# Kernel optimization log

Hardware: AMD Instinct MI355X
Metric: run time of the kernel (lower is better)

The kernel has to match this reference:

```python
import jax, jax.numpy as jnp
import numpy as np

IN_CH = 128
OUT_CH = 128
N_NODES = 50000
N_EDGES = 800000
BN_EPS = 1e-5


def setup_inputs() -> dict:
    key = jax.random.key(0)
    k_x, k_e, k_wl, k_bl, k_wr = jax.random.split(key, 5)
    x = jax.random.normal(k_x, (N_NODES, IN_CH), dtype=jnp.float32)
    edge_index = jax.random.randint(k_e, (2, N_EDGES), 0, N_NODES, dtype=jnp.int64)
    s = 1.0 / np.sqrt(IN_CH)
    W_l = jax.random.uniform(k_wl, (OUT_CH, IN_CH), jnp.float32, -s, s)  # lin_l: aggregated neighbors
    b_l = jax.random.uniform(k_bl, (OUT_CH,), jnp.float32, -s, s)
    W_r = jax.random.uniform(k_wr, (OUT_CH, IN_CH), jnp.float32, -s, s)  # lin_r: root/self
    gamma = jnp.ones((OUT_CH,), jnp.float32)
    beta = jnp.zeros((OUT_CH,), jnp.float32)
    return {"x": x, "edge_index": edge_index, "W_l": W_l, "b_l": b_l,
            "W_r": W_r, "gamma": gamma, "beta": beta}


def reference(x, edge_index, W_l, b_l, W_r, gamma, beta):
    n = x.shape[0]
    src, dst = edge_index[0], edge_index[1]
    # gather source features and mean-aggregate at destination nodes
    msgs = x[src]                                              # [E, C_in]
    agg = jax.ops.segment_sum(msgs, dst, num_segments=n)      # [N, C_in]
    deg = jax.ops.segment_sum(jnp.ones((edge_index.shape[1],), x.dtype), dst, num_segments=n)
    mean_agg = agg / jnp.maximum(deg, 1.0)[:, None]
    # SAGEConv: lin_l(aggregated) + lin_r(self)
    h = mean_agg @ W_l.T + b_l + x @ W_r.T                     # [N, C_out]
    # BatchNorm1d (training-mode batch statistics, biased variance)
    mu = h.mean(axis=0)
    var = ((h - mu) ** 2).mean(axis=0)
    h = (h - mu) * jax.lax.rsqrt(var + BN_EPS) * gamma + beta
    return jax.nn.relu(h)
```

## Files before the change

kernel.cpp:

```cpp
#include <hip/hip_runtime.h>

#define CH 128
#define BN_EPS 1e-5f

typedef unsigned int uint32;
typedef unsigned short ushort16;
using f32x2  = __attribute__((ext_vector_type(2))) float;
using f32x4  = __attribute__((ext_vector_type(4))) float;
using bf16x8 = __attribute__((ext_vector_type(8))) short;

__device__ __forceinline__ ushort16 f2b(float f) {
    uint32 u = __float_as_uint(f);
    return (ushort16)((u + 0x7FFFu + ((u >> 16) & 1u)) >> 16);
}
__device__ __forceinline__ uint32 pk2(float a, float b) {
    return (uint32)f2b(a) | ((uint32)f2b(b) << 16);
}
__device__ __forceinline__ float blo(uint32 u) { return __uint_as_float(u << 16); }
__device__ __forceinline__ float bhi(uint32 u) { return __uint_as_float(u & 0xFFFF0000u); }

__global__ __launch_bounds__(256) void sage_init(
    const float* __restrict__ Wl, const float* __restrict__ Wr,
    int* __restrict__ head, ushort16* __restrict__ wct,
    float* __restrict__ bn, uint32* __restrict__ xqz, int nNodes)
{
    int i = blockIdx.x * 256 + threadIdx.x;
    if (i < nNodes) head[i] = -1;
    if (blockIdx.x < 128) {
        int widx = blockIdx.x * 256 + threadIdx.x;
        int co = widx >> 8, k = widx & 255;
        float v = (k < 128) ? Wr[co * 128 + k] : Wl[co * 128 + (k - 128)];
        wct[widx] = f2b(v);
    }
    if (blockIdx.x == 0) bn[threadIdx.x] = 0.f;
    if (blockIdx.x == 1 && threadIdx.x < 32) xqz[threadIdx.x] = 0;
}

__global__ __launch_bounds__(256) void sage_prep(
    const float* __restrict__ x, const void* __restrict__ ei,
    int* __restrict__ head, int2* __restrict__ pair,
    uint32* __restrict__ xb4, uint2* __restrict__ xq8,
    int nEdges, int total8)
{
    const int* pi = (const int*)ei;
    int lane = threadIdx.x & 63;
    bool is64 = (__ballot(pi[lane * 2 + 1] != 0) == 0ULL);

    int idx = blockIdx.x * 256 + threadIdx.x;
    bool hasE = (idx < nEdges);
    bool hasC = (idx < total8);

    int s = 0, d = 0;
    if (hasE) {
        if (is64) {
            const long long* p = (const long long*)ei;
            s = (int)p[idx];
            d = (int)p[nEdges + idx];
        } else {
            s = pi[idx];
            d = pi[nEdges + idx];
        }
    }
    const float4* x4 = (const float4*)x;
    float4 a = make_float4(0, 0, 0, 0), b = make_float4(0, 0, 0, 0);
    if (hasC) { a = x4[2 * idx]; b = x4[2 * idx + 1]; }

    int old = 0;
    if (hasE) old = atomicExch(&head[d], idx);

    if (hasC) {
        uint4 o;
        o.x = pk2(a.x, a.y); o.y = pk2(a.z, a.w);
        o.z = pk2(b.x, b.y); o.w = pk2(b.z, b.w);
        ((uint4*)xb4)[idx] = o;

        int qa = __builtin_amdgcn_cvt_pk_fp8_f32(a.x, a.y, 0, false);
        qa = __builtin_amdgcn_cvt_pk_fp8_f32(a.z, a.w, qa, true);
        int qb = __builtin_amdgcn_cvt_pk_fp8_f32(b.x, b.y, 0, false);
        qb = __builtin_amdgcn_cvt_pk_fp8_f32(b.z, b.w, qb, true);
        xq8[idx] = make_uint2((uint32)qa, (uint32)qb);
    }

    if (hasE) pair[idx] = make_int2(old, s);
}

__global__ __launch_bounds__(256) void sage_aggregate(
    const char* __restrict__ xq, const int* __restrict__ head,
    const int2* __restrict__ pair, uint32* __restrict__ mean_b, int nNodes)
{
    int wid = blockIdx.x * 4 + (threadIdx.x >> 6);
    int nbase = wid * 8;
    if (nbase >= nNodes) return;
    int lane = threadIdx.x & 63;
    int chain = lane >> 3;
    int sub = lane & 7;

    const int ZROW = nNodes;

    int cur = -1;
    if (lane < 8) {
        int n = nbase + lane;
        cur = (n < nNodes) ? head[n] : -1;
    }
    int cnt = 0;
    f32x2 acc2[8];
    #pragma unroll
    for (int i = 0; i < 8; ++i) acc2[i] = (f32x2){0.f, 0.f};

    int2 pr = make_int2(-1, ZROW);
    if (cur >= 0) pr = pair[cur];

    while (__ballot(cur >= 0) != 0ULL) {
        int nxt = pr.x;
        int2 prn = make_int2(-1, ZROW);
        if (cur >= 0 && nxt >= 0) prn = pair[nxt];

        int s = __shfl(pr.y, chain);
        uint4 u = *(const uint4*)(xq + ((size_t)s << 7) + sub * 16);
        #pragma unroll
        for (int w = 0; w < 4; ++w) {
            uint32 uw = (&u.x)[w];
            acc2[w * 2 + 0] += __builtin_amdgcn_cvt_pk_f32_fp8((int)uw, false);
            acc2[w * 2 + 1] += __builtin_amdgcn_cvt_pk_f32_fp8((int)uw, true);
        }
        if (cur >= 0) { ++cnt; cur = nxt; }
        pr = prn;
    }

    int cn = __shfl(cnt, chain);
    float inv = 1.0f / fmaxf((float)cn, 1.0f);
    int n = nbase + chain;
    if (n < nNodes) {
        uint4 o0 = make_uint4(pk2(acc2[0][0] * inv, acc2[0][1] * inv),
                              pk2(acc2[1][0] * inv, acc2[1][1] * inv),
                              pk2(acc2[2][0] * inv, acc2[2][1] * inv),
                              pk2(acc2[3][0] * inv, acc2[3][1] * inv));
        uint4 o1 = make_uint4(pk2(acc2[4][0] * inv, acc2[4][1] * inv),
                              pk2(acc2[5][0] * inv, acc2[5][1] * inv),
                              pk2(acc2[6][0] * inv, acc2[6][1] * inv),
                              pk2(acc2[7][0] * inv, acc2[7][1] * inv));
        char* base = (char*)mean_b + (size_t)n * 256 + sub * 32;
        *(uint4*)base = o0;
        *(uint4*)(base + 16) = o1;
    }
}

__global__ __launch_bounds__(256) void sage_gemm(
    const ushort16* __restrict__ xb, const ushort16* __restrict__ mean_b,
    const ushort16* __restrict__ wct, const float* __restrict__ bl,
    ushort16* __restrict__ hb, float* __restrict__ bn, int nNodes)
{
    __shared__ ushort16 wsh[8 * 8 * 64 * 8];
    __shared__ float redS[4][CH];
    __shared__ float redQ[4][CH];

    int tid = threadIdx.x;
    int wave = tid >> 6, lane = tid & 63;
    int col = lane & 15, kg = lane >> 4;

    #pragma unroll
    for (int it = 0; it < 16; ++it) {
        int pidx = wave * 16 + it;
        int cb = pidx >> 3, ks = pidx & 7;
        bf16x8 v = *(const bf16x8*)(wct + (size_t)(cb * 16 + col) * 256 + ks * 32 + kg * 8);
        *(bf16x8*)(wsh + ((size_t)pidx * 64 + lane) * 8) = v;
    }

    int row0 = blockIdx.x * 128 + wave * 16;
    int row1 = row0 + 64;
    int arow0 = min(row0 + col, nNodes - 1);
    int arow1 = min(row1 + col, nNodes - 1);
    const ushort16* xr0 = xb + (size_t)arow0 * CH;
    const ushort16* mr0 = mean_b + (size_t)arow0 * CH;
    const ushort16* xr1 = xb + (size_t)arow1 * CH;
    const ushort16* mr1 = mean_b + (size_t)arow1 * CH;

    bf16x8 af0[8], af1[8];
    #pragma unroll
    for (int t = 0; t < 4; ++t) {
        af0[t]     = *(const bf16x8*)(xr0 + t * 32 + kg * 8);
        af0[4 + t] = *(const bf16x8*)(mr0 + t * 32 + kg * 8);
        af1[t]     = *(const bf16x8*)(xr1 + t * 32 + kg * 8);
        af1[4 + t] = *(const bf16x8*)(mr1 + t * 32 + kg * 8);
    }

    __syncthreads();

    f32x4 acc0[8], acc1[8];
    #pragma unroll
    for (int cb = 0; cb < 8; ++cb) {
        acc0[cb] = (f32x4){0.f, 0.f, 0.f, 0.f};
        acc1[cb] = (f32x4){0.f, 0.f, 0.f, 0.f};
    }

    #pragma unroll
    for (int kstep = 0; kstep < 8; ++kstep) {
        #pragma unroll
        for (int cb = 0; cb < 8; ++cb) {
            bf16x8 b = *(const bf16x8*)(wsh + ((size_t)(cb * 8 + kstep) * 64 + lane) * 8);
            acc0[cb] = __builtin_amdgcn_mfma_f32_16x16x32_bf16(af0[kstep], b, acc0[cb], 0, 0, 0);
            acc1[cb] = __builtin_amdgcn_mfma_f32_16x16x32_bf16(af1[kstep], b, acc1[cb], 0, 0, 0);
        }
    }

    #pragma unroll
    for (int cb = 0; cb < 8; ++cb) {
        int co = cb * 16 + col;
        float blv = bl[co];
        float s = 0.f, ss = 0.f;
        #pragma unroll
        for (int j = 0; j < 4; ++j) {
            int r0 = row0 + kg * 4 + j;
            float v0 = acc0[cb][j] + blv;
            if (r0 < nNodes) {
                hb[(size_t)r0 * CH + co] = f2b(v0);
                s += v0; ss += v0 * v0;
            }
            int r1 = row1 + kg * 4 + j;
            float v1 = acc1[cb][j] + blv;
            if (r1 < nNodes) {
                hb[(size_t)r1 * CH + co] = f2b(v1);
                s += v1; ss += v1 * v1;
            }
        }
        s  += __shfl_xor(s, 16);  s  += __shfl_xor(s, 32);
        ss += __shfl_xor(ss, 16); ss += __shfl_xor(ss, 32);
        if (kg == 0) { redS[wave][co] = s; redQ[wave][co] = ss; }
    }
    __syncthreads();
    if (tid < CH) {
        atomicAdd(&bn[tid], redS[0][tid] + redS[1][tid] + redS[2][tid] + redS[3][tid]);
    } else {
        int c = tid - CH;
        atomicAdd(&bn[CH + c], redQ[0][c] + redQ[1][c] + redQ[2][c] + redQ[3][c]);
    }
}

__global__ __launch_bounds__(256) void sage_apply(
    const ushort16* __restrict__ hb, float* __restrict__ out,
    const float* __restrict__ bn, const float* __restrict__ gamma,
    const float* __restrict__ beta, int total8, int nNodes)
{
    __shared__ float sc_sh[CH], sh_sh[CH];
    int tid = threadIdx.x;
    if (tid < CH) {
        float invN = 1.0f / (float)nNodes;
        float mu = bn[tid] * invN;
        float var = fmaxf(bn[CH + tid] * invN - mu * mu, 0.f);
        float sc = gamma[tid] * rsqrtf(var + BN_EPS);
        sc_sh[tid] = sc;
        sh_sh[tid] = beta[tid] - mu * sc;
    }
    __syncthreads();
    int i = blockIdx.x * 256 + tid;
    if (i >= total8) return;
    uint4 u = *(const uint4*)(hb + (size_t)i * 8);
    int c = (i * 8) & 127;
    float4 o0, o1;
    o0.x = fmaxf(fmaf(blo(u.x), sc_sh[c + 0], sh_sh[c + 0]), 0.f);
    o0.y = fmaxf(fmaf(bhi(u.x), sc_sh[c + 1], sh_sh[c + 1]), 0.f);
    o0.z = fmaxf(fmaf(blo(u.y), sc_sh[c + 2], sh_sh[c + 2]), 0.f);
    o0.w = fmaxf(fmaf(bhi(u.y), sc_sh[c + 3], sh_sh[c + 3]), 0.f);
    o1.x = fmaxf(fmaf(blo(u.z), sc_sh[c + 4], sh_sh[c + 4]), 0.f);
    o1.y = fmaxf(fmaf(bhi(u.z), sc_sh[c + 5], sh_sh[c + 5]), 0.f);
    o1.z = fmaxf(fmaf(blo(u.w), sc_sh[c + 6], sh_sh[c + 6]), 0.f);
    o1.w = fmaxf(fmaf(bhi(u.w), sc_sh[c + 7], sh_sh[c + 7]), 0.f);
    float4* dst = (float4*)(out + (size_t)i * 8);
    dst[0] = o0;
    dst[1] = o1;
}

extern "C" void kernel_launch(void* const* d_in, const int* in_sizes, int n_in,
                              void* d_out, int out_size, void* d_ws, size_t ws_size,
                              hipStream_t stream)
{
    const float* x     = (const float*)d_in[0];
    const void*  ei    = d_in[1];
    const float* Wl    = (const float*)d_in[2];
    const float* bl    = (const float*)d_in[3];
    const float* Wr    = (const float*)d_in[4];
    const float* gamma = (const float*)d_in[5];
    const float* beta  = (const float*)d_in[6];

    int nNodes = in_sizes[0] / CH;
    int nEdges = in_sizes[1] / 2;
    int nBlkM  = (nNodes + 127) / 128;

    char* p = (char*)d_ws;
    auto take = [&](size_t bytes) {
        char* r = p;
        p += (bytes + 255) & ~(size_t)255;
        return r;
    };
    ushort16* xb      = (ushort16*)take((size_t)nNodes * CH * 2);
    char*     xq      = (char*)take((size_t)nNodes * CH + 128);
    ushort16* mean_b  = (ushort16*)take((size_t)nNodes * CH * 2);
    ushort16* hb      = (ushort16*)take((size_t)nNodes * CH * 2);
    ushort16* wct     = (ushort16*)take((size_t)CH * 256 * 2);
    int*      head    = (int*)take((size_t)nNodes * 4);
    float*    bn      = (float*)take(256 * 4);
    int2*     pair    = (int2*)take((size_t)nEdges * 8);

    float* out = (float*)d_out;

    int total8 = nNodes * CH / 8;
    int eBlocks = (nEdges + 255) / 256;
    int pBlocks = max(eBlocks, (total8 + 255) / 256);
    int iBlocks = max((nNodes + 255) / 256, 128);

    sage_init<<<iBlocks, 256, 0, stream>>>(
        Wl, Wr, head, wct, bn, (uint32*)(xq + (size_t)nNodes * CH), nNodes);

    sage_prep<<<pBlocks, 256, 0, stream>>>(
        x, ei, head, pair, (uint32*)xb, (uint2*)xq, nEdges, total8);

    int aBlocks = (nNodes + 31) / 32;
    sage_aggregate<<<aBlocks, 256, 0, stream>>>(
        xq, head, pair, (uint32*)mean_b, nNodes);

    sage_gemm<<<nBlkM, 256, 0, stream>>>(
        xb, mean_b, wct, bl, hb, bn, nNodes);

    sage_apply<<<(total8 + 255) / 256, 256, 0, stream>>>(
        hb, out, bn, gamma, beta, total8, nNodes);
}
```

Baseline: 113.7 us.

## Split each node's edge linked list into two chains for more memory parallelism

Edges are now pushed onto one of two per-node linked lists, picked by edge index parity, so each destination has two independent chains. The aggregate kernel walks 16 chains per wave (two per node, in A/B accumulator sets), which halves the serial pointer-chasing depth and doubles the gathers in flight. Partial sums from the two chains are combined with a cross-lane shuffle before the mean is written. This costs twice the head array, doubled accumulator registers, and some idle lanes during the final write.

```diff
diff --git a/kernel.cpp b/kernel.cpp
--- a/kernel.cpp
+++ b/kernel.cpp
@@ -22,10 +22,10 @@
 __global__ __launch_bounds__(256) void sage_init(
     const float* __restrict__ Wl, const float* __restrict__ Wr,
     int* __restrict__ head, ushort16* __restrict__ wct,
-    float* __restrict__ bn, uint32* __restrict__ xqz, int nNodes)
+    float* __restrict__ bn, uint32* __restrict__ xqz, int nHead)
 {
     int i = blockIdx.x * 256 + threadIdx.x;
-    if (i < nNodes) head[i] = -1;
+    if (i < nHead) head[i] = -1;
     if (blockIdx.x < 128) {
         int widx = blockIdx.x * 256 + threadIdx.x;
         int co = widx >> 8, k = widx & 255;
@@ -66,7 +66,7 @@
     if (hasC) { a = x4[2 * idx]; b = x4[2 * idx + 1]; }
 
     int old = 0;
-    if (hasE) old = atomicExch(&head[d], idx);
+    if (hasE) old = atomicExch(&head[(d << 1) | (idx & 1)], idx);
 
     if (hasC) {
         uint4 o;
@@ -92,20 +92,20 @@
     int nbase = wid * 8;
     if (nbase >= nNodes) return;
     int lane = threadIdx.x & 63;
-    int chain = lane >> 3;
+    int grp = lane >> 3;
     int sub = lane & 7;
 
     const int ZROW = nNodes;
 
     int cur = -1;
-    if (lane < 8) {
-        int n = nbase + lane;
-        cur = (n < nNodes) ? head[n] : -1;
+    if (lane < 16) {
+        int n = nbase + (lane >> 1);
+        if (n < nNodes) cur = head[((size_t)n << 1) | (lane & 1)];
     }
     int cnt = 0;
-    f32x2 acc2[8];
-    #pragma unroll
-    for (int i = 0; i < 8; ++i) acc2[i] = (f32x2){0.f, 0.f};
+    f32x2 aA[8], aB[8];
+    #pragma unroll
+    for (int i = 0; i < 8; ++i) { aA[i] = (f32x2){0.f, 0.f}; aB[i] = (f32x2){0.f, 0.f}; }
 
     int2 pr = make_int2(-1, ZROW);
     if (cur >= 0) pr = pair[cur];
@@ -115,33 +115,63 @@
         int2 prn = make_int2(-1, ZROW);
         if (cur >= 0 && nxt >= 0) prn = pair[nxt];
 
-        int s = __shfl(pr.y, chain);
-        uint4 u = *(const uint4*)(xq + ((size_t)s << 7) + sub * 16);
+        int sA = __shfl(pr.y, grp);
+        int sB = __shfl(pr.y, 8 + grp);
+        uint4 uA = *(const uint4*)(xq + ((size_t)sA << 7) + sub * 16);
+        uint4 uB = *(const uint4*)(xq + ((size_t)sB << 7) + sub * 16);
         #pragma unroll
         for (int w = 0; w < 4; ++w) {
-            uint32 uw = (&u.x)[w];
-            acc2[w * 2 + 0] += __builtin_amdgcn_cvt_pk_f32_fp8((int)uw, false);
-            acc2[w * 2 + 1] += __builtin_amdgcn_cvt_pk_f32_fp8((int)uw, true);
+            uint32 wA = (&uA.x)[w], wB = (&uB.x)[w];
+            aA[w * 2 + 0] += __builtin_amdgcn_cvt_pk_f32_fp8((int)wA, false);
+            aA[w * 2 + 1] += __builtin_amdgcn_cvt_pk_f32_fp8((int)wA, true);
+            aB[w * 2 + 0] += __builtin_amdgcn_cvt_pk_f32_fp8((int)wB, false);
+            aB[w * 2 + 1] += __builtin_amdgcn_cvt_pk_f32_fp8((int)wB, true);
         }
         if (cur >= 0) { ++cnt; cur = nxt; }
         pr = prn;
     }
 
-    int cn = __shfl(cnt, chain);
-    float inv = 1.0f / fmaxf((float)cn, 1.0f);
-    int n = nbase + chain;
-    if (n < nNodes) {
-        uint4 o0 = make_uint4(pk2(acc2[0][0] * inv, acc2[0][1] * inv),
-                              pk2(acc2[1][0] * inv, acc2[1][1] * inv),
-                              pk2(acc2[2][0] * inv, acc2[2][1] * inv),
-                              pk2(acc2[3][0] * inv, acc2[3][1] * inv));
-        uint4 o1 = make_uint4(pk2(acc2[4][0] * inv, acc2[4][1] * inv),
-                              pk2(acc2[5][0] * inv, acc2[5][1] * inv),
-                              pk2(acc2[6][0] * inv, acc2[6][1] * inv),
-                              pk2(acc2[7][0] * inv, acc2[7][1] * inv));
-        char* base = (char*)mean_b + (size_t)n * 256 + sub * 32;
-        *(uint4*)base = o0;
-        *(uint4*)(base + 16) = o1;
+    #pragma unroll
+    for (int i = 0; i < 8; ++i) {
+        aA[i][0] += __shfl_xor(aA[i][0], 8);
+        aA[i][1] += __shfl_xor(aA[i][1], 8);
+        aB[i][0] += __shfl_xor(aB[i][0], 8);
+        aB[i][1] += __shfl_xor(aB[i][1], 8);
+    }
+    int cA = __shfl(cnt, grp & ~1) + __shfl(cnt, grp | 1);
+    int cB = __shfl(cnt, 8 + (grp & ~1)) + __shfl(cnt, 8 + (grp | 1));
+
+    if ((grp & 1) == 0) {
+        float invA = 1.0f / fmaxf((float)cA, 1.0f);
+        int nA = nbase + (grp >> 1);
+        if (nA < nNodes) {
+            uint4 o0 = make_uint4(pk2(aA[0][0] * invA, aA[0][1] * invA),
+                                  pk2(aA[1][0] * invA, aA[1][1] * invA),
+                                  pk2(aA[2][0] * invA, aA[2][1] * invA),
+                                  pk2(aA[3][0] * invA, aA[3][1] * invA));
+            uint4 o1 = make_uint4(pk2(aA[4][0] * invA, aA[4][1] * invA),
+                                  pk2(aA[5][0] * invA, aA[5][1] * invA),
+                                  pk2(aA[6][0] * invA, aA[6][1] * invA),
+                                  pk2(aA[7][0] * invA, aA[7][1] * invA));
+            char* base = (char*)mean_b + (size_t)nA * 256 + sub * 32;
+            *(uint4*)base = o0;
+            *(uint4*)(base + 16) = o1;
+        }
+        float invB = 1.0f / fmaxf((float)cB, 1.0f);
+        int nB = nbase + 4 + (grp >> 1);
+        if (nB < nNodes) {
+            uint4 o0 = make_uint4(pk2(aB[0][0] * invB, aB[0][1] * invB),
+                                  pk2(aB[1][0] * invB, aB[1][1] * invB),
+                                  pk2(aB[2][0] * invB, aB[2][1] * invB),
+                                  pk2(aB[3][0] * invB, aB[3][1] * invB));
+            uint4 o1 = make_uint4(pk2(aB[4][0] * invB, aB[4][1] * invB),
+                                  pk2(aB[5][0] * invB, aB[5][1] * invB),
+                                  pk2(aB[6][0] * invB, aB[6][1] * invB),
+                                  pk2(aB[7][0] * invB, aB[7][1] * invB));
+            char* base = (char*)mean_b + (size_t)nB * 256 + sub * 32;
+            *(uint4*)base = o0;
+            *(uint4*)(base + 16) = o1;
+        }
     }
 }
 
@@ -284,6 +314,7 @@
 
     int nNodes = in_sizes[0] / CH;
     int nEdges = in_sizes[1] / 2;
+    int nHead  = nNodes * 2;
     int nBlkM  = (nNodes + 127) / 128;
 
     char* p = (char*)d_ws;
@@ -297,7 +328,7 @@
     ushort16* mean_b  = (ushort16*)take((size_t)nNodes * CH * 2);
     ushort16* hb      = (ushort16*)take((size_t)nNodes * CH * 2);
     ushort16* wct     = (ushort16*)take((size_t)CH * 256 * 2);
-    int*      head    = (int*)take((size_t)nNodes * 4);
+    int*      head    = (int*)take((size_t)nHead * 4);
     float*    bn      = (float*)take(256 * 4);
     int2*     pair    = (int2*)take((size_t)nEdges * 8);
 
@@ -306,10 +337,10 @@
     int total8 = nNodes * CH / 8;
     int eBlocks = (nEdges + 255) / 256;
     int pBlocks = max(eBlocks, (total8 + 255) / 256);
-    int iBlocks = max((nNodes + 255) / 256, 128);
+    int iBlocks = max((nHead + 255) / 256, 128);
 
     sage_init<<<iBlocks, 256, 0, stream>>>(
-        Wl, Wr, head, wct, bn, (uint32*)(xq + (size_t)nNodes * CH), nNodes);
+        Wl, Wr, head, wct, bn, (uint32*)(xq + (size_t)nNodes * CH), nHead);
 
     sage_prep<<<pBlocks, 256, 0, stream>>>(
         x, ei, head, pair, (uint32*)xb, (uint2*)xq, nEdges, total8);
```

Result: slower. 119.7 us (+5.2%).
